# Performance work log

Measured on AMD Instinct MI355X. Metric: run time of the kernel, lower is better.

The kernel has to match this reference:

```python
import jax, jax.numpy as jnp
import numpy as np

N = 100000        # nodes
E = 1600000       # edges
NFEAT = 500
NHID = [256, 128]
NCLASS = 40
K = 10
ALPHA = 0.1


def setup_inputs() -> dict:
    key = jax.random.key(0)
    ks = jax.random.split(key, 9)
    x = jax.random.normal(ks[0], (N, NFEAT), dtype=jnp.float32)
    edge_index = jax.random.randint(ks[1], (2, E), 0, N, dtype=jnp.int32)
    dims = [NFEAT] + NHID + [NCLASS]
    # Linear params (PyTorch convention: W is [out, in])
    W0 = jax.random.normal(ks[2], (dims[1], dims[0]), jnp.float32) / np.sqrt(dims[0])
    b0 = jnp.zeros((dims[1],), jnp.float32)
    W1 = jax.random.normal(ks[3], (dims[2], dims[1]), jnp.float32) / np.sqrt(dims[1])
    b1 = jnp.zeros((dims[2],), jnp.float32)
    W2 = jax.random.normal(ks[4], (dims[3], dims[2]), jnp.float32) / np.sqrt(dims[2])
    b2 = jnp.zeros((dims[3],), jnp.float32)
    return {"x": x, "edge_index": edge_index,
            "W0": W0, "b0": b0, "W1": W1, "b1": b1, "W2": W2, "b2": b2}


def reference(x, edge_index, W0, b0, W1, b1, W2, b2):
    # MLP encoder: ReLU after every Linear (dropout is identity in eval mode)
    h = x
    for W, b in ((W0, b0), (W1, b1), (W2, b2)):
        h = jax.nn.relu(h @ W.T + b)   # [N, out]

    # --- APPNP propagation with GCN normalization (self-loops added) ---
    loops = jnp.arange(N, dtype=edge_index.dtype)
    src = jnp.concatenate([edge_index[0], loops])  # [E+N]
    dst = jnp.concatenate([edge_index[1], loops])  # [E+N]
    deg = jnp.zeros((N,), h.dtype).at[dst].add(jnp.ones_like(dst, h.dtype))
    dinv = jax.lax.rsqrt(deg)                      # deg >= 1 due to self-loops
    norm = dinv[src] * dinv[dst]                   # [E+N]

    h0 = h
    for _ in range(K):
        msg = h[src] * norm[:, None]               # gather + scale, [E+N, C]
        agg = jnp.zeros_like(h).at[dst].add(msg)   # scatter-add, [N, C]
        h = (1.0 - ALPHA) * agg + ALPHA * h0       # teleport fusion
    return h
```

## Files before the change

### kernel.cpp

```cpp
#include <hip/hip_runtime.h>

#define NN 100000
#define EE 1600000
#define KITER 10

typedef __attribute__((ext_vector_type(8))) short s16x8;
typedef __attribute__((ext_vector_type(4))) float f32x4;

__device__ __forceinline__ short f2bf(float f) {
    union { float f; unsigned u; } v; v.f = f;
    unsigned r = v.u + 0x7FFFu + ((v.u >> 16) & 1u);
    return (short)(r >> 16);
}

__device__ __forceinline__ void gload_lds16(const void* g, void* l) {
    __builtin_amdgcn_global_load_lds(
        (const __attribute__((address_space(1))) void*)g,
        (__attribute__((address_space(3))) void*)l, 16, 0, 0);
}

template<int KSTEPS, bool OUT_BF16>
__global__ __launch_bounds__(256)
void mfma_gemm(const short* __restrict__ A, int lda, const short* __restrict__ B,
               const float* __restrict__ bias, int nbias,
               void* __restrict__ Cout, int ldc, int ncols_store, int nrows)
{
    __shared__ short ldsA[128 * 32];
    __shared__ short ldsB[128 * 32];
    const int t    = threadIdx.x;
    const int lane = t & 63;
    const int wid  = t >> 6;
    const int rowBase = blockIdx.y * 128;
    const int colBase = blockIdx.x * 128;
    const int wrow = (wid >> 1) * 64;
    const int wcol = (wid & 1) * 64;

    const int q  = t & 3;
    const int rl = t >> 2;

    f32x4 acc[4][4] = {};
    const int KPB = KSTEPS * 32;

    for (int ks = 0; ks < KSTEPS; ++ks) {
        const int k0 = ks * 32;

        #pragma unroll
        for (int i = 0; i < 2; ++i) {
            const short* srcB = B + (size_t)(colBase + rl + i * 64) * KPB + k0 + q * 8;
            gload_lds16(srcB, &ldsB[wid * 512 + i * 2048]);
        }
        #pragma unroll
        for (int i = 0; i < 2; ++i) {
            int grow = rowBase + rl + i * 64; if (grow > NN - 1) grow = NN - 1;
            const short* srcA = A + (size_t)grow * lda + k0 + q * 8;
            gload_lds16(srcA, &ldsA[wid * 512 + i * 2048]);
        }

        __syncthreads();

        {
            const int kb = lane >> 4;
            const int l16 = lane & 15;
            s16x8 a[4], b[4];
            #pragma unroll
            for (int m = 0; m < 4; ++m)
                a[m] = *(const s16x8*)&ldsA[(wrow + m * 16 + l16) * 32 + kb * 8];
            #pragma unroll
            for (int n = 0; n < 4; ++n)
                b[n] = *(const s16x8*)&ldsB[(wcol + n * 16 + l16) * 32 + kb * 8];
            #pragma unroll
            for (int m = 0; m < 4; ++m)
                #pragma unroll
                for (int n = 0; n < 4; ++n)
                    acc[m][n] = __builtin_amdgcn_mfma_f32_16x16x32_bf16(
                        a[m], b[n], acc[m][n], 0, 0, 0);
        }

        __syncthreads();
    }

    const int crow0 = (lane >> 4) * 4;
    const int ccol  = lane & 15;
    #pragma unroll
    for (int n = 0; n < 4; ++n) {
        int col = colBase + wcol + n * 16 + ccol;
        float bv = (col < nbias) ? bias[col] : 0.f;
        #pragma unroll
        for (int m = 0; m < 4; ++m) {
            #pragma unroll
            for (int j = 0; j < 4; ++j) {
                int row = rowBase + wrow + m * 16 + crow0 + j;
                if (row >= nrows) continue;
                float v = acc[m][n][j] + bv;
                v = fmaxf(v, 0.f);
                if (OUT_BF16) {
                    ((short*)Cout)[(size_t)row * ldc + col] = f2bf(v);
                } else if (col < ncols_store) {
                    ((float*)Cout)[(size_t)row * ldc + col] = v;
                }
            }
        }
    }
}

__global__ void convert_x_kernel(const float* __restrict__ in, short* __restrict__ out) {
    int idx = blockIdx.x * blockDim.x + threadIdx.x;
    if (idx >= (NN * 500) / 8) return;
    const float4* in4 = (const float4*)in;
    float4 a = in4[(size_t)idx * 2];
    float4 b = in4[(size_t)idx * 2 + 1];
    s16x8 s;
    s[0]=f2bf(a.x); s[1]=f2bf(a.y); s[2]=f2bf(a.z); s[3]=f2bf(a.w);
    s[4]=f2bf(b.x); s[5]=f2bf(b.y); s[6]=f2bf(b.z); s[7]=f2bf(b.w);
    *(s16x8*)&out[(size_t)idx * 8] = s;
}

__global__ void convert_w_kernel(const float* __restrict__ in, short* __restrict__ out,
                                 int R, int C, int Rp, int Cp) {
    int idx = blockIdx.x * blockDim.x + threadIdx.x;
    if (idx >= Rp * Cp) return;
    int r = idx / Cp, c = idx - r * Cp;
    float v = (r < R && c < C) ? in[r * C + c] : 0.f;
    out[idx] = f2bf(v);
}

__global__ void deg_init_kernel(int* deg, int n) {
    int i = blockIdx.x * blockDim.x + threadIdx.x;
    if (i < n) deg[i] = 1;
}
__global__ void deg_count_kernel(const int* __restrict__ dst, int* deg, int e) {
    int i = blockIdx.x * blockDim.x + threadIdx.x;
    if (i < e) atomicAdd(&deg[dst[i]], 1);
}
__global__ void dinv_kernel(const int* __restrict__ deg, float* __restrict__ dinv,
                            float* __restrict__ dinv2, int n) {
    int i = blockIdx.x * blockDim.x + threadIdx.x;
    if (i < n) {
        float d = (float)deg[i];
        dinv[i] = rsqrtf(d);
        dinv2[i] = 1.0f / d;
    }
}
__global__ __launch_bounds__(256)
void scan1_kernel(const int* __restrict__ deg, int* __restrict__ row_ptr,
                  int* __restrict__ blockSums, int n) {
    __shared__ int sdata[256];
    const int base = blockIdx.x * 2048;
    const int t = threadIdx.x;
    int local[8];
    int s = 0;
    #pragma unroll
    for (int i = 0; i < 8; ++i) {
        int idx = base + t * 8 + i;
        int c = (idx < n) ? (deg[idx] - 1) : 0;
        local[i] = s;
        s += c;
    }
    sdata[t] = s;
    __syncthreads();
    for (int off = 1; off < 256; off <<= 1) {
        int v = (t >= off) ? sdata[t - off] : 0;
        __syncthreads();
        sdata[t] += v;
        __syncthreads();
    }
    int excl = (t == 0) ? 0 : sdata[t - 1];
    #pragma unroll
    for (int i = 0; i < 8; ++i) {
        int idx = base + t * 8 + i;
        if (idx < n) row_ptr[idx] = excl + local[i];
    }
    if (t == 255) blockSums[blockIdx.x] = sdata[255];
}
__global__ void scan2_kernel(int* blockSums, int nb) {
    if (threadIdx.x == 0 && blockIdx.x == 0) {
        int s = 0;
        for (int i = 0; i < nb; ++i) { int v = blockSums[i]; blockSums[i] = s; s += v; }
    }
}
__global__ void scan3_kernel(int* __restrict__ row_ptr, int* __restrict__ cursor,
                             const int* __restrict__ blockSums, int n, int e) {
    int i = blockIdx.x * blockDim.x + threadIdx.x;
    if (i < n) {
        int v = row_ptr[i] + blockSums[i >> 11];
        row_ptr[i] = v;
        cursor[i] = v;
    }
    if (i == 0) row_ptr[n] = e;
}
__global__ void fill_csr_kernel(const int* __restrict__ src, const int* __restrict__ dst,
                                const float* __restrict__ dinv, int* cursor,
                                int2* __restrict__ pairs, int e) {
    int i = blockIdx.x * blockDim.x + threadIdx.x;
    if (i < e) {
        int s = src[i], d = dst[i];
        int pos = atomicAdd(&cursor[d], 1);
        float nv = dinv[s] * dinv[d];
        pairs[pos] = make_int2(s, __float_as_int(nv));
    }
}

__global__ __launch_bounds__(320)
void prop_kernel(const float4* __restrict__ hin4, const float4* __restrict__ h04,
                 const int* __restrict__ rowp, const int2* __restrict__ pairs,
                 const float* __restrict__ dinv2, float4* __restrict__ hout4, int n)
{
    const int t = threadIdx.x;
    const int vl = t / 10;
    const int f4 = t - vl * 10;
    const int v = blockIdx.x * 32 + vl;
    if (v >= n) return;
    const size_t base = (size_t)v * 10 + f4;

    float4 sf = hin4[base];
    const float dv = dinv2[v];
    float ax = dv * sf.x, ay = dv * sf.y, az = dv * sf.z, aw = dv * sf.w;

    int e = rowp[v];
    const int e1 = rowp[v + 1];

    for (; e + 8 <= e1; e += 8) {
        int2 p0 = pairs[e],     p1 = pairs[e + 1], p2 = pairs[e + 2], p3 = pairs[e + 3];
        int2 p4 = pairs[e + 4], p5 = pairs[e + 5], p6 = pairs[e + 6], p7 = pairs[e + 7];
        float4 g0 = hin4[(size_t)p0.x * 10 + f4];
        float4 g1 = hin4[(size_t)p1.x * 10 + f4];
        float4 g2 = hin4[(size_t)p2.x * 10 + f4];
        float4 g3 = hin4[(size_t)p3.x * 10 + f4];
        float4 g4 = hin4[(size_t)p4.x * 10 + f4];
        float4 g5 = hin4[(size_t)p5.x * 10 + f4];
        float4 g6 = hin4[(size_t)p6.x * 10 + f4];
        float4 g7 = hin4[(size_t)p7.x * 10 + f4];
        float w0 = __int_as_float(p0.y), w1 = __int_as_float(p1.y);
        float w2 = __int_as_float(p2.y), w3 = __int_as_float(p3.y);
        float w4 = __int_as_float(p4.y), w5 = __int_as_float(p5.y);
        float w6 = __int_as_float(p6.y), w7 = __int_as_float(p7.y);
        ax = fmaf(w0, g0.x, ax); ay = fmaf(w0, g0.y, ay); az = fmaf(w0, g0.z, az); aw = fmaf(w0, g0.w, aw);
        ax = fmaf(w1, g1.x, ax); ay = fmaf(w1, g1.y, ay); az = fmaf(w1, g1.z, az); aw = fmaf(w1, g1.w, aw);
        ax = fmaf(w2, g2.x, ax); ay = fmaf(w2, g2.y, ay); az = fmaf(w2, g2.z, az); aw = fmaf(w2, g2.w, aw);
        ax = fmaf(w3, g3.x, ax); ay = fmaf(w3, g3.y, ay); az = fmaf(w3, g3.z, az); aw = fmaf(w3, g3.w, aw);
        ax = fmaf(w4, g4.x, ax); ay = fmaf(w4, g4.y, ay); az = fmaf(w4, g4.z, az); aw = fmaf(w4, g4.w, aw);
        ax = fmaf(w5, g5.x, ax); ay = fmaf(w5, g5.y, ay); az = fmaf(w5, g5.z, az); aw = fmaf(w5, g5.w, aw);
        ax = fmaf(w6, g6.x, ax); ay = fmaf(w6, g6.y, ay); az = fmaf(w6, g6.z, az); aw = fmaf(w6, g6.w, aw);
        ax = fmaf(w7, g7.x, ax); ay = fmaf(w7, g7.y, ay); az = fmaf(w7, g7.z, az); aw = fmaf(w7, g7.w, aw);
    }
    for (; e < e1; ++e) {
        int2 p = pairs[e];
        float4 g = hin4[(size_t)p.x * 10 + f4];
        float w = __int_as_float(p.y);
        ax = fmaf(w, g.x, ax); ay = fmaf(w, g.y, ay);
        az = fmaf(w, g.z, az); aw = fmaf(w, g.w, aw);
    }

    float4 h0v = h04[base];
    float4 o;
    o.x = fmaf(0.9f, ax, 0.1f * h0v.x);
    o.y = fmaf(0.9f, ay, 0.1f * h0v.y);
    o.z = fmaf(0.9f, az, 0.1f * h0v.z);
    o.w = fmaf(0.9f, aw, 0.1f * h0v.w);
    hout4[base] = o;
}

extern "C" void kernel_launch(void* const* d_in, const int* in_sizes, int n_in,
                              void* d_out, int out_size, void* d_ws, size_t ws_size,
                              hipStream_t stream) {
    const float* x  = (const float*)d_in[0];
    const int* ei   = (const int*)d_in[1];
    const float* W0 = (const float*)d_in[2];
    const float* b0 = (const float*)d_in[3];
    const float* W1 = (const float*)d_in[4];
    const float* b1 = (const float*)d_in[5];
    const float* W2 = (const float*)d_in[6];
    const float* b2 = (const float*)d_in[7];
    float* out = (float*)d_out;
    char* ws = (char*)d_ws;

    const int* src = ei;
    const int* dst = ei + EE;

    short* xb   = (short*)(ws);
    short* h1b  = (short*)(ws + 100000000);
    short* W0b  = (short*)(ws + 151200000);
    short* W1b  = (short*)(ws + 151462144);
    short* W2b  = (short*)(ws + 151527680);

    short* h2b  = (short*)(ws);
    float* h0   = (float*)(ws + 25600000);
    float* hA   = (float*)(ws + 41600000);
    float* hB   = (float*)(ws + 57600000);

    int2*  pairs= (int2*) (ws + 100000000);
    int*   deg  = (int*)  (ws + 112800000);
    float* dinv = (float*)(ws + 113200000);
    float* dnv2 = (float*)(ws + 113600000);
    int*   rowp = (int*)  (ws + 114000000);
    int*   curs = (int*)  (ws + 114400008);
    int*   bsum = (int*)  (ws + 114800008);
    (void)ws_size; (void)in_sizes; (void)n_in; (void)out_size;

    convert_x_kernel<<<((NN * 500 / 8) + 255) / 256, 256, 0, stream>>>(x, xb);
    convert_w_kernel<<<(256 * 512 + 255) / 256, 256, 0, stream>>>(W0, W0b, 256, 500, 256, 512);
    convert_w_kernel<<<(128 * 256 + 255) / 256, 256, 0, stream>>>(W1, W1b, 128, 256, 128, 256);
    convert_w_kernel<<<(128 * 128 + 255) / 256, 256, 0, stream>>>(W2, W2b, 40, 128, 128, 128);

    const int NBLK = (NN + 127) / 128;
    mfma_gemm<16, true ><<<dim3(2, NBLK), 256, 0, stream>>>(
        xb, 500, W0b, b0, 256, (void*)h1b, 256, 256, NN);
    mfma_gemm<8,  true ><<<dim3(1, NBLK), 256, 0, stream>>>(
        h1b, 256, W1b, b1, 128, (void*)h2b, 128, 128, NN);
    mfma_gemm<4,  false><<<dim3(1, NBLK), 256, 0, stream>>>(
        h2b, 128, W2b, b2, 40, (void*)h0, 40, 40, NN);

    {
        int nb_n = (NN + 255) / 256;
        int nb_e = (EE + 255) / 256;
        deg_init_kernel<<<nb_n, 256, 0, stream>>>(deg, NN);
        deg_count_kernel<<<nb_e, 256, 0, stream>>>(dst, deg, EE);
        dinv_kernel<<<nb_n, 256, 0, stream>>>(deg, dinv, dnv2, NN);
        int nb_scan = (NN + 2047) / 2048;
        scan1_kernel<<<nb_scan, 256, 0, stream>>>(deg, rowp, bsum, NN);
        scan2_kernel<<<1, 64, 0, stream>>>(bsum, nb_scan);
        scan3_kernel<<<nb_n, 256, 0, stream>>>(rowp, curs, bsum, NN, EE);
        fill_csr_kernel<<<nb_e, 256, 0, stream>>>(src, dst, dinv, curs, pairs, EE);
    }

    {
        dim3 blk(320);
        dim3 grd((NN + 31) / 32);
        const float* hin = h0;
        for (int it = 0; it < KITER; ++it) {
            float* hout = (it == KITER - 1) ? out : ((it & 1) ? hB : hA);
            prop_kernel<<<grd, blk, 0, stream>>>(
                (const float4*)hin, (const float4*)h0, rowp, pairs, dnv2,
                (float4*)hout, NN);
            hin = hout;
        }
    }
}
```

Before: 912.1 us.

## Store propagation features in bf16 to halve gather traffic

The APPNP propagation now keeps the intermediate node features in bf16 instead of fp32, so each 16-byte gather fetches 8 features rather than 4. Each thread handles 8 features and a block handles 64 nodes. The final GEMM writes a bf16 copy for propagation plus an fp32 copy of h0 for the teleport term, and the last iteration writes fp32 output. Rounding to bf16 at every iteration adds error that builds up over the 10 steps.

```diff
diff --git a/kernel.cpp b/kernel.cpp
--- a/kernel.cpp
+++ b/kernel.cpp
@@ -12,6 +12,9 @@
     unsigned r = v.u + 0x7FFFu + ((v.u >> 16) & 1u);
     return (short)(r >> 16);
 }
+__device__ __forceinline__ float bf2f(short s) {
+    return __uint_as_float((unsigned)(unsigned short)s << 16);
+}
 
 __device__ __forceinline__ void gload_lds16(const void* g, void* l) {
     __builtin_amdgcn_global_load_lds(
@@ -23,7 +26,8 @@
 __global__ __launch_bounds__(256)
 void mfma_gemm(const short* __restrict__ A, int lda, const short* __restrict__ B,
                const float* __restrict__ bias, int nbias,
-               void* __restrict__ Cout, int ldc, int ncols_store, int nrows)
+               void* __restrict__ Cout, int ldc, int ncols_store, int nrows,
+               float* __restrict__ C2)
 {
     __shared__ short ldsA[128 * 32];
     __shared__ short ldsB[128 * 32];
@@ -93,10 +97,12 @@
                 if (row >= nrows) continue;
                 float v = acc[m][n][j] + bv;
                 v = fmaxf(v, 0.f);
-                if (OUT_BF16) {
-                    ((short*)Cout)[(size_t)row * ldc + col] = f2bf(v);
-                } else if (col < ncols_store) {
-                    ((float*)Cout)[(size_t)row * ldc + col] = v;
+                if (col < ncols_store) {
+                    if (OUT_BF16)
+                        ((short*)Cout)[(size_t)row * ldc + col] = f2bf(v);
+                    else
+                        ((float*)Cout)[(size_t)row * ldc + col] = v;
+                    if (C2) C2[(size_t)row * ldc + col] = v;
                 }
             }
         }
@@ -201,20 +207,24 @@
 }
 
 __global__ __launch_bounds__(320)
-void prop_kernel(const float4* __restrict__ hin4, const float4* __restrict__ h04,
-                 const int* __restrict__ rowp, const int2* __restrict__ pairs,
-                 const float* __restrict__ dinv2, float4* __restrict__ hout4, int n)
+void prop_bf16_kernel(const short* __restrict__ hin, const float* __restrict__ h0f,
+                      const int* __restrict__ rowp, const int2* __restrict__ pairs,
+                      const float* __restrict__ dinv2,
+                      short* __restrict__ hout, float* __restrict__ outF, int n)
 {
     const int t = threadIdx.x;
-    const int vl = t / 10;
-    const int f4 = t - vl * 10;
-    const int v = blockIdx.x * 32 + vl;
+    const int vl = t / 5;
+    const int f = t - vl * 5;
+    const int v = blockIdx.x * 64 + vl;
     if (v >= n) return;
-    const size_t base = (size_t)v * 10 + f4;
-
-    float4 sf = hin4[base];
-    const float dv = dinv2[v];
-    float ax = dv * sf.x, ay = dv * sf.y, az = dv * sf.z, aw = dv * sf.w;
+
+    float acc[8];
+    {
+        const float dv = dinv2[v];
+        s16x8 s = *(const s16x8*)(hin + (size_t)v * 40 + f * 8);
+        #pragma unroll
+        for (int j = 0; j < 8; ++j) acc[j] = dv * bf2f(s[j]);
+    }
 
     int e = rowp[v];
     const int e1 = rowp[v + 1];
@@ -222,42 +232,58 @@
     for (; e + 8 <= e1; e += 8) {
         int2 p0 = pairs[e],     p1 = pairs[e + 1], p2 = pairs[e + 2], p3 = pairs[e + 3];
         int2 p4 = pairs[e + 4], p5 = pairs[e + 5], p6 = pairs[e + 6], p7 = pairs[e + 7];
-        float4 g0 = hin4[(size_t)p0.x * 10 + f4];
-        float4 g1 = hin4[(size_t)p1.x * 10 + f4];
-        float4 g2 = hin4[(size_t)p2.x * 10 + f4];
-        float4 g3 = hin4[(size_t)p3.x * 10 + f4];
-        float4 g4 = hin4[(size_t)p4.x * 10 + f4];
-        float4 g5 = hin4[(size_t)p5.x * 10 + f4];
-        float4 g6 = hin4[(size_t)p6.x * 10 + f4];
-        float4 g7 = hin4[(size_t)p7.x * 10 + f4];
+        s16x8 g0 = *(const s16x8*)(hin + (size_t)p0.x * 40 + f * 8);
+        s16x8 g1 = *(const s16x8*)(hin + (size_t)p1.x * 40 + f * 8);
+        s16x8 g2 = *(const s16x8*)(hin + (size_t)p2.x * 40 + f * 8);
+        s16x8 g3 = *(const s16x8*)(hin + (size_t)p3.x * 40 + f * 8);
+        s16x8 g4 = *(const s16x8*)(hin + (size_t)p4.x * 40 + f * 8);
+        s16x8 g5 = *(const s16x8*)(hin + (size_t)p5.x * 40 + f * 8);
+        s16x8 g6 = *(const s16x8*)(hin + (size_t)p6.x * 40 + f * 8);
+        s16x8 g7 = *(const s16x8*)(hin + (size_t)p7.x * 40 + f * 8);
         float w0 = __int_as_float(p0.y), w1 = __int_as_float(p1.y);
         float w2 = __int_as_float(p2.y), w3 = __int_as_float(p3.y);
         float w4 = __int_as_float(p4.y), w5 = __int_as_float(p5.y);
         float w6 = __int_as_float(p6.y), w7 = __int_as_float(p7.y);
-        ax = fmaf(w0, g0.x, ax); ay = fmaf(w0, g0.y, ay); az = fmaf(w0, g0.z, az); aw = fmaf(w0, g0.w, aw);
-        ax = fmaf(w1, g1.x, ax); ay = fmaf(w1, g1.y, ay); az = fmaf(w1, g1.z, az); aw = fmaf(w1, g1.w, aw);
-        ax = fmaf(w2, g2.x, ax); ay = fmaf(w2, g2.y, ay); az = fmaf(w2, g2.z, az); aw = fmaf(w2, g2.w, aw);
-        ax = fmaf(w3, g3.x, ax); ay = fmaf(w3, g3.y, ay); az = fmaf(w3, g3.z, az); aw = fmaf(w3, g3.w, aw);
-        ax = fmaf(w4, g4.x, ax); ay = fmaf(w4, g4.y, ay); az = fmaf(w4, g4.z, az); aw = fmaf(w4, g4.w, aw);
-        ax = fmaf(w5, g5.x, ax); ay = fmaf(w5, g5.y, ay); az = fmaf(w5, g5.z, az); aw = fmaf(w5, g5.w, aw);
-        ax = fmaf(w6, g6.x, ax); ay = fmaf(w6, g6.y, ay); az = fmaf(w6, g6.z, az); aw = fmaf(w6, g6.w, aw);
-        ax = fmaf(w7, g7.x, ax); ay = fmaf(w7, g7.y, ay); az = fmaf(w7, g7.z, az); aw = fmaf(w7, g7.w, aw);
+        #pragma unroll
+        for (int j = 0; j < 8; ++j) acc[j] = fmaf(w0, bf2f(g0[j]), acc[j]);
+        #pragma unroll
+        for (int j = 0; j < 8; ++j) acc[j] = fmaf(w1, bf2f(g1[j]), acc[j]);
+        #pragma unroll
+        for (int j = 0; j < 8; ++j) acc[j] = fmaf(w2, bf2f(g2[j]), acc[j]);
+        #pragma unroll
+        for (int j = 0; j < 8; ++j) acc[j] = fmaf(w3, bf2f(g3[j]), acc[j]);
+        #pragma unroll
+        for (int j = 0; j < 8; ++j) acc[j] = fmaf(w4, bf2f(g4[j]), acc[j]);
+        #pragma unroll
+        for (int j = 0; j < 8; ++j) acc[j] = fmaf(w5, bf2f(g5[j]), acc[j]);
+        #pragma unroll
+        for (int j = 0; j < 8; ++j) acc[j] = fmaf(w6, bf2f(g6[j]), acc[j]);
+        #pragma unroll
+        for (int j = 0; j < 8; ++j) acc[j] = fmaf(w7, bf2f(g7[j]), acc[j]);
     }
     for (; e < e1; ++e) {
         int2 p = pairs[e];
-        float4 g = hin4[(size_t)p.x * 10 + f4];
+        s16x8 g = *(const s16x8*)(hin + (size_t)p.x * 40 + f * 8);
         float w = __int_as_float(p.y);
-        ax = fmaf(w, g.x, ax); ay = fmaf(w, g.y, ay);
-        az = fmaf(w, g.z, az); aw = fmaf(w, g.w, aw);
-    }
-
-    float4 h0v = h04[base];
-    float4 o;
-    o.x = fmaf(0.9f, ax, 0.1f * h0v.x);
-    o.y = fmaf(0.9f, ay, 0.1f * h0v.y);
-    o.z = fmaf(0.9f, az, 0.1f * h0v.z);
-    o.w = fmaf(0.9f, aw, 0.1f * h0v.w);
-    hout4[base] = o;
+        #pragma unroll
+        for (int j = 0; j < 8; ++j) acc[j] = fmaf(w, bf2f(g[j]), acc[j]);
+    }
+
+    const float* h0p = h0f + (size_t)v * 40 + f * 8;
+    float o[8];
+    #pragma unroll
+    for (int j = 0; j < 8; ++j) o[j] = fmaf(0.9f, acc[j], 0.1f * h0p[j]);
+
+    if (outF) {
+        float4* op = (float4*)(outF + (size_t)v * 40 + f * 8);
+        op[0] = make_float4(o[0], o[1], o[2], o[3]);
+        op[1] = make_float4(o[4], o[5], o[6], o[7]);
+    } else {
+        s16x8 s;
+        #pragma unroll
+        for (int j = 0; j < 8; ++j) s[j] = f2bf(o[j]);
+        *(s16x8*)(hout + (size_t)v * 40 + f * 8) = s;
+    }
 }
 
 extern "C" void kernel_launch(void* const* d_in, const int* in_sizes, int n_in,
@@ -284,9 +310,10 @@
     short* W2b  = (short*)(ws + 151527680);
 
     short* h2b  = (short*)(ws);
-    float* h0   = (float*)(ws + 25600000);
-    float* hA   = (float*)(ws + 41600000);
-    float* hB   = (float*)(ws + 57600000);
+    short* h0b  = (short*)(ws + 25600000);
+    float* h0f  = (float*)(ws + 33600000);
+    short* hA   = (short*)(ws + 49600000);
+    short* hB   = (short*)(ws + 57600000);
 
     int2*  pairs= (int2*) (ws + 100000000);
     int*   deg  = (int*)  (ws + 112800000);
@@ -304,11 +331,11 @@
 
     const int NBLK = (NN + 127) / 128;
     mfma_gemm<16, true ><<<dim3(2, NBLK), 256, 0, stream>>>(
-        xb, 500, W0b, b0, 256, (void*)h1b, 256, 256, NN);
+        xb, 500, W0b, b0, 256, (void*)h1b, 256, 256, NN, nullptr);
     mfma_gemm<8,  true ><<<dim3(1, NBLK), 256, 0, stream>>>(
-        h1b, 256, W1b, b1, 128, (void*)h2b, 128, 128, NN);
-    mfma_gemm<4,  false><<<dim3(1, NBLK), 256, 0, stream>>>(
-        h2b, 128, W2b, b2, 40, (void*)h0, 40, 40, NN);
+        h1b, 256, W1b, b1, 128, (void*)h2b, 128, 128, NN, nullptr);
+    mfma_gemm<4,  true ><<<dim3(1, NBLK), 256, 0, stream>>>(
+        h2b, 128, W2b, b2, 40, (void*)h0b, 40, 40, NN, h0f);
 
     {
         int nb_n = (NN + 255) / 256;
@@ -325,13 +352,13 @@
 
     {
         dim3 blk(320);
-        dim3 grd((NN + 31) / 32);
-        const float* hin = h0;
+        dim3 grd((NN + 63) / 64);
+        const short* hin = h0b;
         for (int it = 0; it < KITER; ++it) {
-            float* hout = (it == KITER - 1) ? out : ((it & 1) ? hB : hA);
-            prop_kernel<<<grd, blk, 0, stream>>>(
-                (const float4*)hin, (const float4*)h0, rowp, pairs, dnv2,
-                (float4*)hout, NN);
+            short* hout = (it & 1) ? hB : hA;
+            float* fin  = (it == KITER - 1) ? out : nullptr;
+            prop_bf16_kernel<<<grd, blk, 0, stream>>>(
+                hin, h0f, rowp, pairs, dnv2, hout, fin, NN);
             hin = hout;
         }
     }
```

New measurement: 756.1 us, median of 2. 17.1% less time.
